# Kernel tuning notes

Measured on AMD Instinct MI355X. Metric: run time of the kernel, lower is better.

Reference implementation:

```python
import jax, jax.numpy as jnp
import numpy as np

EPS = 1e-7  # Keras K.epsilon()
ATT_DIM = 50

def setup_inputs() -> dict:
    key = jax.random.key(0)
    k1, k2, k3, k4 = jax.random.split(key, 4)
    B, T, D = 64, 4096, 256
    x = jax.random.normal(k1, (B, T, D), dtype=jnp.float32)
    # RandomNormal init (stddev default 0.05 in keras RandomNormal)
    W = 0.05 * jax.random.normal(k2, (D, ATT_DIM), dtype=jnp.float32)
    b = 0.05 * jax.random.normal(k3, (ATT_DIM,), dtype=jnp.float32)
    u = 0.05 * jax.random.normal(k4, (ATT_DIM, 1), dtype=jnp.float32)
    return {"x": x, "W": W, "b": b, "u": u}

def reference(x, W, b, u):
    # uit: [B, T, A]
    uit = jnp.tanh(jnp.einsum('btd,da->bta', x, W) + b)
    # ait: [B, T]  (no max-subtraction, faithful to K.exp then normalize)
    ait = jnp.exp(jnp.einsum('bta,a->bt', uit, u[:, 0]))
    ait = ait / (jnp.sum(ait, axis=1, keepdims=True) + EPS)
    # weighted sum pooling over seq axis -> [B, D]
    return jnp.einsum('btd,bt->bd', x, ait)
```

## Files before the change

### kernel.cpp

```cpp
#include <hip/hip_runtime.h>
#include <stdint.h>

#define B_    64
#define T_    4096
#define D_    256
#define A_    50
#define APAD  64
#define TB    256
#define ST    32
#define WT_STRIDE 264
#define XS_STRIDE 264
#define EPS_  1e-7f

#define OFF_NUM 0
#define OFF_DEN 16384
#define OFF_B   16448
#define OFF_U   16512
#define OFF_WT  16576

typedef __attribute__((ext_vector_type(8))) short short8;
typedef __attribute__((ext_vector_type(4))) float floatx4;

__device__ __forceinline__ unsigned short f32_to_bf16(float f) {
    union { float f; uint32_t u; } v; v.f = f;
    uint32_t u = v.u;
    uint32_t r = u + 0x7FFFu + ((u >> 16) & 1u);
    return (unsigned short)(r >> 16);
}

__device__ __forceinline__ float fast_tanh(float x) {
    float e2 = __expf(2.0f * x);
    return (e2 - 1.0f) * __builtin_amdgcn_rcpf(e2 + 1.0f);
}

__global__ void att_prologue(const float* __restrict__ W,
                             const float* __restrict__ bias,
                             const float* __restrict__ u,
                             float* __restrict__ ws) {
    int idx = blockIdx.x * blockDim.x + threadIdx.x;
    int stride = gridDim.x * blockDim.x;
    for (int i = idx; i < OFF_DEN + B_; i += stride) ws[i] = 0.0f;
    for (int i = idx; i < APAD; i += stride) {
        ws[OFF_B + i] = (i < A_) ? bias[i] : 0.0f;
        ws[OFF_U + i] = (i < A_) ? u[i]    : 0.0f;
    }
    unsigned short* wt = (unsigned short*)(ws + OFF_WT);
    for (int i = idx; i < APAD * D_; i += stride) {
        int a = i >> 8;
        int k = i & 255;
        float val = (a < A_) ? W[k * A_ + a] : 0.0f;
        wt[a * WT_STRIDE + k] = f32_to_bf16(val);
    }
}

__global__ __launch_bounds__(256, 4) void att_main(const float* __restrict__ x,
                                                   float* __restrict__ ws) {
    __shared__ unsigned short lds_x[ST * XS_STRIDE];
    __shared__ float part[ST][4];
    __shared__ float e_lds[ST];

    const int tid  = threadIdx.x;
    const int wave = tid >> 6;
    const int lane = tid & 63;
    const int bb   = blockIdx.y;
    const int tblk = blockIdx.x;

    const float* xblk = x + ((size_t)bb * T_ + (size_t)tblk * TB) * D_;

    float4 r[8];
    {
        const float4* xg = (const float4*)xblk;
        #pragma unroll
        for (int i = 0; i < 4; ++i) {
            r[2 * i]     = xg[2 * tid + 512 * i];
            r[2 * i + 1] = xg[2 * tid + 512 * i + 1];
        }
    }

    short8 bw[8];
    {
        const unsigned short* wt = (const unsigned short*)(ws + OFF_WT);
        const unsigned short* wrow = wt + (wave * 16 + (lane & 15)) * WT_STRIDE
                                        + ((lane >> 4) * 8);
        #pragma unroll
        for (int ks = 0; ks < 8; ++ks)
            bw[ks] = *(const short8*)(wrow + ks * 32);
    }

    const int c = wave * 16 + (lane & 15);
    const float b_c = ws[OFF_B + c];
    const float u_c = ws[OFF_U + c];

    float num_acc = 0.0f;
    float den_acc = 0.0f;

    const int arow0 = (lane & 15) * XS_STRIDE;
    const int arow1 = (16 + (lane & 15)) * XS_STRIDE;
    const int koff  = (lane >> 4) * 8;
    const int wrow_lds = (tid >> 5) * XS_STRIDE + (tid & 31) * 8;

    for (int st = 0; st < TB / ST; ++st) {
        __syncthreads();

        #pragma unroll
        for (int i = 0; i < 4; ++i) {
            uint4 p;
            p.x = ((uint32_t)f32_to_bf16(r[2*i].y)   << 16) | f32_to_bf16(r[2*i].x);
            p.y = ((uint32_t)f32_to_bf16(r[2*i].w)   << 16) | f32_to_bf16(r[2*i].z);
            p.z = ((uint32_t)f32_to_bf16(r[2*i+1].y) << 16) | f32_to_bf16(r[2*i+1].x);
            p.w = ((uint32_t)f32_to_bf16(r[2*i+1].w) << 16) | f32_to_bf16(r[2*i+1].z);
            *(uint4*)&lds_x[wrow_lds + i * 8 * XS_STRIDE] = p;
        }
        __syncthreads();

        if (st < TB / ST - 1) {
            const float4* xn = (const float4*)(xblk + (st + 1) * ST * D_);
            #pragma unroll
            for (int i = 0; i < 4; ++i) {
                r[2 * i]     = xn[2 * tid + 512 * i];
                r[2 * i + 1] = xn[2 * tid + 512 * i + 1];
            }
        }

        floatx4 acc0 = {0.f, 0.f, 0.f, 0.f};
        floatx4 acc1 = {0.f, 0.f, 0.f, 0.f};
        #pragma unroll
        for (int ks = 0; ks < 8; ++ks) {
            short8 a0 = *(const short8*)&lds_x[arow0 + ks * 32 + koff];
            short8 a1 = *(const short8*)&lds_x[arow1 + ks * 32 + koff];
            acc0 = __builtin_amdgcn_mfma_f32_16x16x32_bf16(a0, bw[ks], acc0, 0, 0, 0);
            acc1 = __builtin_amdgcn_mfma_f32_16x16x32_bf16(a1, bw[ks], acc1, 0, 0, 0);
        }

        float lp0[4], lp1[4];
        #pragma unroll
        for (int rr = 0; rr < 4; ++rr) {
            float v0 = fast_tanh(acc0[rr] + b_c) * u_c;
            float v1 = fast_tanh(acc1[rr] + b_c) * u_c;
            v0 += __shfl_xor(v0, 1); v1 += __shfl_xor(v1, 1);
            v0 += __shfl_xor(v0, 2); v1 += __shfl_xor(v1, 2);
            v0 += __shfl_xor(v0, 4); v1 += __shfl_xor(v1, 4);
            v0 += __shfl_xor(v0, 8); v1 += __shfl_xor(v1, 8);
            lp0[rr] = v0; lp1[rr] = v1;
        }
        if ((lane & 15) == 0) {
            int rg = lane >> 4;
            #pragma unroll
            for (int rr = 0; rr < 4; ++rr) {
                part[rg * 4 + rr][wave]      = lp0[rr];
                part[16 + rg * 4 + rr][wave] = lp1[rr];
            }
        }
        __syncthreads();

        if (tid < ST) {
            float ev = __expf(part[tid][0] + part[tid][1] + part[tid][2] + part[tid][3]);
            e_lds[tid] = ev;
            den_acc += ev;
        }
        __syncthreads();

        #pragma unroll
        for (int t = 0; t < ST; ++t) {
            float xv = __uint_as_float((uint32_t)lds_x[t * XS_STRIDE + tid] << 16);
            num_acc = fmaf(xv, e_lds[t], num_acc);
        }
    }

    atomicAdd(&ws[OFF_NUM + bb * D_ + tid], num_acc);
    if (wave == 0) {
        float v = den_acc;
        v += __shfl_xor(v, 32);
        v += __shfl_xor(v, 16);
        v += __shfl_xor(v, 8);
        v += __shfl_xor(v, 4);
        v += __shfl_xor(v, 2);
        v += __shfl_xor(v, 1);
        if (lane == 0) atomicAdd(&ws[OFF_DEN + bb], v);
    }
}

__global__ void att_epilogue(const float* __restrict__ ws, float* __restrict__ out) {
    int bb = blockIdx.x;
    int d  = threadIdx.x;
    out[bb * D_ + d] = ws[OFF_NUM + bb * D_ + d] / (ws[OFF_DEN + bb] + EPS_);
}

extern "C" void kernel_launch(void* const* d_in, const int* in_sizes, int n_in,
                              void* d_out, int out_size, void* d_ws, size_t ws_size,
                              hipStream_t stream) {
    const float* x = (const float*)d_in[0];
    const float* W = (const float*)d_in[1];
    const float* b = (const float*)d_in[2];
    const float* u = (const float*)d_in[3];
    float* ws  = (float*)d_ws;
    float* out = (float*)d_out;

    att_prologue<<<64, 256, 0, stream>>>(W, b, u, ws);
    att_main<<<dim3(T_ / TB, B_), 256, 0, stream>>>(x, ws);
    att_epilogue<<<B_, 256, 0, stream>>>(ws, out);
}
```

Measured before the change: 367.0 us.

## Keep packed x tile in registers for pooling and drop a barrier per subtile

```diff
diff --git a/kernel.cpp b/kernel.cpp
--- a/kernel.cpp
+++ b/kernel.cpp
@@ -8,6 +8,7 @@
 #define APAD  64
 #define TB    256
 #define ST    32
+#define NSUB  (TB / ST)
 #define WT_STRIDE 264
 #define XS_STRIDE 264
 #define EPS_  1e-7f
@@ -32,6 +33,18 @@
     float e2 = __expf(2.0f * x);
     return (e2 - 1.0f) * __builtin_amdgcn_rcpf(e2 + 1.0f);
 }
+
+__device__ __forceinline__ uint4 pack8(const float4 a, const float4 b) {
+    uint4 p;
+    p.x = ((uint32_t)f32_to_bf16(a.y) << 16) | f32_to_bf16(a.x);
+    p.y = ((uint32_t)f32_to_bf16(a.w) << 16) | f32_to_bf16(a.z);
+    p.z = ((uint32_t)f32_to_bf16(b.y) << 16) | f32_to_bf16(b.x);
+    p.w = ((uint32_t)f32_to_bf16(b.w) << 16) | f32_to_bf16(b.z);
+    return p;
+}
+
+__device__ __forceinline__ float bf_lo(uint32_t w) { return __uint_as_float(w << 16); }
+__device__ __forceinline__ float bf_hi(uint32_t w) { return __uint_as_float(w & 0xFFFF0000u); }
 
 __global__ void att_prologue(const float* __restrict__ W,
                              const float* __restrict__ bias,
@@ -55,9 +68,8 @@
 
 __global__ __launch_bounds__(256, 4) void att_main(const float* __restrict__ x,
                                                    float* __restrict__ ws) {
-    __shared__ unsigned short lds_x[ST * XS_STRIDE];
-    __shared__ float part[ST][4];
-    __shared__ float e_lds[ST];
+    __shared__ __align__(16) unsigned short lds_x[ST * XS_STRIDE];
+    __shared__ __align__(16) float part[ST][4];
 
     const int tid  = threadIdx.x;
     const int wave = tid >> 6;
@@ -67,16 +79,6 @@
 
     const float* xblk = x + ((size_t)bb * T_ + (size_t)tblk * TB) * D_;
 
-    float4 r[8];
-    {
-        const float4* xg = (const float4*)xblk;
-        #pragma unroll
-        for (int i = 0; i < 4; ++i) {
-            r[2 * i]     = xg[2 * tid + 512 * i];
-            r[2 * i + 1] = xg[2 * tid + 512 * i + 1];
-        }
-    }
-
     short8 bw[8];
     {
         const unsigned short* wt = (const unsigned short*)(ws + OFF_WT);
@@ -91,34 +93,49 @@
     const float b_c = ws[OFF_B + c];
     const float u_c = ws[OFF_U + c];
 
-    float num_acc = 0.0f;
-    float den_acc = 0.0f;
-
+    const int g = tid >> 5;
+    const int m = tid & 31;
     const int arow0 = (lane & 15) * XS_STRIDE;
     const int arow1 = (16 + (lane & 15)) * XS_STRIDE;
     const int koff  = (lane >> 4) * 8;
-    const int wrow_lds = (tid >> 5) * XS_STRIDE + (tid & 31) * 8;
-
-    for (int st = 0; st < TB / ST; ++st) {
-        __syncthreads();
-
+    const int wrow_lds = g * XS_STRIDE + m * 8;
+
+    float np[8];
+    #pragma unroll
+    for (int j = 0; j < 8; ++j) np[j] = 0.0f;
+    float den_acc = 0.0f;
+
+    uint4 rbuf[2][4];
+
+    {
+        const float4* xg = (const float4*)xblk;
+        float4 t[8];
         #pragma unroll
         for (int i = 0; i < 4; ++i) {
-            uint4 p;
-            p.x = ((uint32_t)f32_to_bf16(r[2*i].y)   << 16) | f32_to_bf16(r[2*i].x);
-            p.y = ((uint32_t)f32_to_bf16(r[2*i].w)   << 16) | f32_to_bf16(r[2*i].z);
-            p.z = ((uint32_t)f32_to_bf16(r[2*i+1].y) << 16) | f32_to_bf16(r[2*i+1].x);
-            p.w = ((uint32_t)f32_to_bf16(r[2*i+1].w) << 16) | f32_to_bf16(r[2*i+1].z);
+            t[2 * i]     = xg[2 * tid + 512 * i];
+            t[2 * i + 1] = xg[2 * tid + 512 * i + 1];
+        }
+        #pragma unroll
+        for (int i = 0; i < 4; ++i) {
+            uint4 p = pack8(t[2 * i], t[2 * i + 1]);
+            rbuf[0][i] = p;
             *(uint4*)&lds_x[wrow_lds + i * 8 * XS_STRIDE] = p;
         }
-        __syncthreads();
-
-        if (st < TB / ST - 1) {
-            const float4* xn = (const float4*)(xblk + (st + 1) * ST * D_);
-            #pragma unroll
-            for (int i = 0; i < 4; ++i) {
-                r[2 * i]     = xn[2 * tid + 512 * i];
-                r[2 * i + 1] = xn[2 * tid + 512 * i + 1];
+    }
+    __syncthreads();
+
+    #pragma unroll
+    for (int st = 0; st < NSUB; ++st) {
+        const int cur = st & 1;
+        const int nxt = cur ^ 1;
+
+        float4 t[8];
+        const float4* xn = (const float4*)(xblk + (st + 1) * ST * D_);
+        if (st < NSUB - 1) {
+            #pragma unroll
+            for (int i = 0; i < 2; ++i) {
+                t[2 * i]     = xn[2 * tid + 512 * i];
+                t[2 * i + 1] = xn[2 * tid + 512 * i + 1];
             }
         }
 
@@ -130,6 +147,14 @@
             short8 a1 = *(const short8*)&lds_x[arow1 + ks * 32 + koff];
             acc0 = __builtin_amdgcn_mfma_f32_16x16x32_bf16(a0, bw[ks], acc0, 0, 0, 0);
             acc1 = __builtin_amdgcn_mfma_f32_16x16x32_bf16(a1, bw[ks], acc1, 0, 0, 0);
+        }
+
+        if (st < NSUB - 1) {
+            #pragma unroll
+            for (int i = 2; i < 4; ++i) {
+                t[2 * i]     = xn[2 * tid + 512 * i];
+                t[2 * i + 1] = xn[2 * tid + 512 * i + 1];
+            }
         }
 
         float lp0[4], lp1[4];
@@ -153,21 +178,45 @@
         }
         __syncthreads();
 
+        #pragma unroll
+        for (int i = 0; i < 4; ++i) {
+            const float4 pp = *(const float4*)part[g + 8 * i];
+            const float ev = __expf(pp.x + pp.y + pp.z + pp.w);
+            const uint4 p = rbuf[cur][i];
+            np[0] = fmaf(bf_lo(p.x), ev, np[0]);
+            np[1] = fmaf(bf_hi(p.x), ev, np[1]);
+            np[2] = fmaf(bf_lo(p.y), ev, np[2]);
+            np[3] = fmaf(bf_hi(p.y), ev, np[3]);
+            np[4] = fmaf(bf_lo(p.z), ev, np[4]);
+            np[5] = fmaf(bf_hi(p.z), ev, np[5]);
+            np[6] = fmaf(bf_lo(p.w), ev, np[6]);
+            np[7] = fmaf(bf_hi(p.w), ev, np[7]);
+        }
         if (tid < ST) {
-            float ev = __expf(part[tid][0] + part[tid][1] + part[tid][2] + part[tid][3]);
-            e_lds[tid] = ev;
-            den_acc += ev;
-        }
-        __syncthreads();
-
-        #pragma unroll
-        for (int t = 0; t < ST; ++t) {
-            float xv = __uint_as_float((uint32_t)lds_x[t * XS_STRIDE + tid] << 16);
-            num_acc = fmaf(xv, e_lds[t], num_acc);
-        }
-    }
-
-    atomicAdd(&ws[OFF_NUM + bb * D_ + tid], num_acc);
+            const float4 pp = *(const float4*)part[tid];
+            den_acc += __expf(pp.x + pp.y + pp.z + pp.w);
+        }
+
+        if (st < NSUB - 1) {
+            #pragma unroll
+            for (int i = 0; i < 4; ++i) {
+                uint4 p = pack8(t[2 * i], t[2 * i + 1]);
+                rbuf[nxt][i] = p;
+                *(uint4*)&lds_x[wrow_lds + i * 8 * XS_STRIDE] = p;
+            }
+            __syncthreads();
+        }
+    }
+
+    float* red = (float*)lds_x;
+    *(float4*)&red[g * D_ + m * 8]     = make_float4(np[0], np[1], np[2], np[3]);
+    *(float4*)&red[g * D_ + m * 8 + 4] = make_float4(np[4], np[5], np[6], np[7]);
+    __syncthreads();
+    float s = 0.0f;
+    #pragma unroll
+    for (int gg = 0; gg < 8; ++gg) s += red[gg * D_ + tid];
+    atomicAdd(&ws[OFF_NUM + bb * D_ + tid], s);
+
     if (wave == 0) {
         float v = den_acc;
         v += __shfl_xor(v, 32);
```

Measured after the change: 410.8 us. 1.12x slower.
